# Kernel tuning notes

Measured on AMD Instinct MI355X. Metric: run time of the kernel, lower is better.

The kernel has to match this reference:

```python
import jax, jax.numpy as jnp
import numpy as np

K = 512          # num_embeddings
D = 8            # latent_dim
DECAY = 0.99     # ema_decay
EPS = 1e-5


def setup_inputs() -> dict:
    key = jax.random.key(0)
    k1, k2 = jax.random.split(key)
    z = jax.random.normal(k1, (64, D, 64, 64), dtype=jnp.float32)
    # codebook initialized uniform(-1/K, 1/K) as in the torch module
    codebook = jax.random.uniform(k2, (K, D), dtype=jnp.float32,
                                  minval=-1.0 / K, maxval=1.0 / K)
    ema_cluster_size = jnp.zeros((K,), dtype=jnp.float32)
    ema_w = jnp.zeros((K, D), dtype=jnp.float32)
    return {"z": z, "codebook": codebook,
            "ema_cluster_size": ema_cluster_size, "ema_w": ema_w}


def reference(z, codebook, ema_cluster_size, ema_w):
    B, C, H, W = z.shape
    # (B, HW, C) flattened latents, matching z.view(B,C,-1).permute(0,2,1)
    flat = z.reshape(B, C, H * W).transpose(0, 2, 1)

    # cdist p=2: ||z||^2 - 2 z.e + ||e||^2, then sqrt (argmin unaffected,
    # but we keep the sqrt for faithfulness to torch.cdist)
    z_sq = jnp.sum(flat * flat, axis=-1, keepdims=True)        # (B, N, 1)
    e_sq = jnp.sum(codebook * codebook, axis=-1)               # (K,)
    dots = jnp.einsum('bnd,kd->bnk', flat, codebook)           # (B, N, K)
    distances = jnp.sqrt(jnp.maximum(z_sq - 2.0 * dots + e_sq, 0.0))

    indices = jnp.argmin(distances, axis=-1)                   # (B, N) int

    # embedding gather with the OLD codebook (as in the torch forward)
    z_q = codebook[indices]                                    # (B, N, D)
    z_q = z_q.transpose(0, 2, 1).reshape(B, C, H, W)

    commitment_loss = jnp.mean((jax.lax.stop_gradient(z_q) - z) ** 2)
    loss = commitment_loss  # use_ema=True branch

    # ---- EMA in-place codebook update (buffers) ----
    idx_flat = indices.reshape(-1)                             # (B*N,)
    inp_flat = flat.reshape(-1, C)                             # (B*N, D)
    counts = jax.ops.segment_sum(jnp.ones_like(idx_flat, dtype=z.dtype),
                                 idx_flat, num_segments=K)     # (K,)
    sums = jax.ops.segment_sum(inp_flat, idx_flat, num_segments=K)  # (K, D)

    new_cs = ema_cluster_size * DECAY + counts * (1.0 - DECAY)
    new_w = ema_w * DECAY + sums * (1.0 - DECAY)
    n = jnp.sum(new_cs)
    cs_smoothed = (new_cs + EPS) / (n + K * EPS) * n
    new_codebook = new_w / cs_smoothed[:, None]

    return z_q, loss, new_codebook, cs_smoothed, new_w
```

## Files before the change

kernel.cpp:

```cpp
#include <hip/hip_runtime.h>

constexpr int Kc   = 512;
constexpr int Dc   = 8;
constexpr int HWc  = 4096;
constexpr int CHWc = Dc * HWc;
constexpr int Mc   = 64 * HWc;
constexpr int TOTALc = Mc * Dc;

constexpr int REP      = 8;
constexpr int RSTRIDE  = 4616;
constexpr int ACC_FLOATS = REP * RSTRIDE;

__global__ __launch_bounds__(256) void vq_prep(const float* __restrict__ cb,
                                               float* __restrict__ ws) {
    const int tid = blockIdx.x * 256 + threadIdx.x;
    float4* w4 = (float4*)ws;
    for (int i = tid; i < ACC_FLOATS / 4; i += gridDim.x * 256)
        w4[i] = float4{0.f, 0.f, 0.f, 0.f};
    if (blockIdx.x == 0) {
        for (int k = threadIdx.x; k < Kc; k += 256) {
            float s = 0.f;
#pragma unroll
            for (int c = 0; c < Dc; ++c) {
                const float e = cb[k * Dc + c];
                s = fmaf(e, e, s);
            }
            ws[ACC_FLOATS + k] = s;
        }
    }
}

__global__ __launch_bounds__(512, 8) void vq_main(const float* __restrict__ z,
                                                  const float* __restrict__ cb,
                                                  const float* __restrict__ esq,
                                                  float* __restrict__ ws,
                                                  float* __restrict__ zq) {
    __shared__ float s_counts[Kc];
    __shared__ float s_sums[Kc * Dc];
    __shared__ float s_mn[512];
    __shared__ int   s_im[512];
    __shared__ float s_loss;

    const int t = threadIdx.x;
    for (int i = t; i < Kc; i += 512) s_counts[i] = 0.f;
    for (int i = t; i < Kc * Dc; i += 512) s_sums[i] = 0.f;
    if (t == 0) s_loss = 0.f;

    const int v = t & 255;
    const int half = __builtin_amdgcn_readfirstlane(t >> 8);
    const int k0   = half << 8;

    const int m = blockIdx.x * 256 + v;
    const int n = m & (HWc - 1);
    const int b = m >> 12;
    const float* zb = z + b * CHWc + n;

    float zv[Dc], zz[Dc];
#pragma unroll
    for (int c = 0; c < Dc; ++c) {
        zv[c] = zb[c * HWc];
        zz[c] = -2.0f * zv[c];
    }

    float mn = 3.4e38f;
    int   im = k0;
#pragma unroll 4
    for (int kk = 0; kk < 256; ++kk) {
        const int k = k0 + kk;
        float a = esq[k];
#pragma unroll
        for (int c = 0; c < Dc; ++c) {
            const float e = cb[k * Dc + c];
            a = fmaf(zz[c], e, a);
        }
        const bool cm = a < mn;
        mn = cm ? a : mn;
        im = cm ? k : im;
    }
    s_mn[t] = mn;
    s_im[t] = im;
    __syncthreads();

    if (t < 256) {
        const float mn0 = s_mn[t];
        const float mn1 = s_mn[t + 256];
        const int   im0 = s_im[t];
        const int   im1 = s_im[t + 256];
        const int im = (mn1 < mn0) ? im1 : im0;

        const float4* cb4 = (const float4*)cb;
        const float4 qa = cb4[im * 2], qb = cb4[im * 2 + 1];
        const float q[Dc] = {qa.x, qa.y, qa.z, qa.w, qb.x, qb.y, qb.z, qb.w};

        float* zqb = zq + b * CHWc + n;
        float lsum = 0.f;
#pragma unroll
        for (int c = 0; c < Dc; ++c) {
            zqb[c * HWc] = q[c];
            const float d = q[c] - zv[c];
            lsum = fmaf(d, d, lsum);
        }

        unsafeAtomicAdd(&s_counts[im], 1.0f);
#pragma unroll
        for (int c = 0; c < Dc; ++c)
            unsafeAtomicAdd(&s_sums[im * Dc + c], zv[c]);
        unsafeAtomicAdd(&s_loss, lsum);
    }
    __syncthreads();

    float* acc = ws + (blockIdx.x & (REP - 1)) * RSTRIDE;
    for (int i = t; i < Kc; i += 512) {
        const float val = s_counts[i];
        if (val != 0.f) unsafeAtomicAdd(&acc[i], val);
    }
    for (int i = t; i < Kc * Dc; i += 512) {
        const float val = s_sums[i];
        if (val != 0.f) unsafeAtomicAdd(&acc[512 + i], val);
    }
    if (t == 0) unsafeAtomicAdd(&acc[4608], s_loss);
}

__global__ __launch_bounds__(512) void vq_final(const float* __restrict__ ws,
                                                const float* __restrict__ ema_cs,
                                                const float* __restrict__ ema_w,
                                                float* __restrict__ out) {
    constexpr float DEC  = 0.99f;
    constexpr float OMD  = (float)(1.0 - 0.99);
    constexpr float EPSf = 1e-5f;
    constexpr float KEPS = (float)(512 * 1e-5);
    __shared__ float red[512];

    const int k = threadIdx.x;
    float cnt = 0.f;
#pragma unroll
    for (int r = 0; r < REP; ++r) cnt += ws[r * RSTRIDE + k];
    const float ncs = ema_cs[k] * DEC + cnt * OMD;
    red[k] = ncs;
    __syncthreads();
    for (int s = 256; s > 0; s >>= 1) {
        if (k < s) red[k] += red[k + s];
        __syncthreads();
    }
    const float n  = red[0];
    const float cs = (ncs + EPSf) / (n + KEPS) * n;

    float* out_loss = out + TOTALc;
    float* out_cb   = out + TOTALc + 1;
    float* out_cs   = out_cb + Kc * Dc;
    float* out_nw   = out_cs + Kc;

    out_cs[k] = cs;
#pragma unroll
    for (int c = 0; c < Dc; ++c) {
        float sm = 0.f;
#pragma unroll
        for (int r = 0; r < REP; ++r) sm += ws[r * RSTRIDE + 512 + k * Dc + c];
        const float nw = ema_w[k * Dc + c] * DEC + sm * OMD;
        out_nw[k * Dc + c] = nw;
        out_cb[k * Dc + c] = nw / cs;
    }
    if (k == 0) {
        float ls = 0.f;
#pragma unroll
        for (int r = 0; r < REP; ++r) ls += ws[r * RSTRIDE + 4608];
        out_loss[0] = ls * (1.0f / 2097152.0f);
    }
}

extern "C" void kernel_launch(void* const* d_in, const int* in_sizes, int n_in,
                              void* d_out, int out_size, void* d_ws, size_t ws_size,
                              hipStream_t stream) {
    const float* z      = (const float*)d_in[0];
    const float* cb     = (const float*)d_in[1];
    const float* ema_cs = (const float*)d_in[2];
    const float* ema_w  = (const float*)d_in[3];
    float* out = (float*)d_out;
    float* ws  = (float*)d_ws;

    vq_prep<<<32, 256, 0, stream>>>(cb, ws);
    vq_main<<<Mc / 256, 512, 0, stream>>>(z, cb, ws + ACC_FLOATS, ws, out);
    vq_final<<<1, 512, 0, stream>>>(ws, ema_cs, ema_w, out);
}
```

Before: 129.3 us.

## Register-block two latents per thread and split codebook into four groups

The main kernel now has each thread evaluate two latent vectors against a 128-entry slice of the codebook, with four thread groups covering all 512 codes, instead of one vector against 256 codes across two groups. Each codebook element loaded is therefore reused for two FMAs, cutting cache and LDS traffic per distance. The partial argmins are combined over four groups in shared memory, and z is reloaded in the epilogue rather than kept in registers. The finalize kernel also switches to coalesced element-wise loops over the sums, with cluster sizes shared through LDS.

```diff
diff --git a/kernel.cpp b/kernel.cpp
--- a/kernel.cpp
+++ b/kernel.cpp
@@ -37,8 +37,8 @@
                                                   float* __restrict__ zq) {
     __shared__ float s_counts[Kc];
     __shared__ float s_sums[Kc * Dc];
-    __shared__ float s_mn[512];
-    __shared__ int   s_im[512];
+    __shared__ float s_mn[4][256];
+    __shared__ int   s_im[4][256];
     __shared__ float s_loss;
 
     const int t = threadIdx.x;
@@ -46,65 +46,82 @@
     for (int i = t; i < Kc * Dc; i += 512) s_sums[i] = 0.f;
     if (t == 0) s_loss = 0.f;
 
-    const int v = t & 255;
-    const int half = __builtin_amdgcn_readfirstlane(t >> 8);
-    const int k0   = half << 8;
-
-    const int m = blockIdx.x * 256 + v;
-    const int n = m & (HWc - 1);
-    const int b = m >> 12;
-    const float* zb = z + b * CHWc + n;
-
-    float zv[Dc], zz[Dc];
+    const int vl = t & 127;
+    const int g  = __builtin_amdgcn_readfirstlane(t >> 7);
+    const int k0 = g << 7;
+
+    const int base = blockIdx.x * 256;
+    const int n0 = (base + vl) & (HWc - 1);
+    const int b  = base >> 12;
+    const float* zb = z + b * CHWc + n0;
+
+    float zz0[Dc], zz1[Dc];
 #pragma unroll
     for (int c = 0; c < Dc; ++c) {
-        zv[c] = zb[c * HWc];
-        zz[c] = -2.0f * zv[c];
-    }
-
-    float mn = 3.4e38f;
-    int   im = k0;
+        zz0[c] = -2.0f * zb[c * HWc];
+        zz1[c] = -2.0f * zb[c * HWc + 128];
+    }
+
+    float mn0 = 3.4e38f, mn1 = 3.4e38f;
+    int   i0 = k0, i1 = k0;
 #pragma unroll 4
-    for (int kk = 0; kk < 256; ++kk) {
+    for (int kk = 0; kk < 128; ++kk) {
         const int k = k0 + kk;
-        float a = esq[k];
+        float a0 = esq[k];
+        float a1 = a0;
 #pragma unroll
         for (int c = 0; c < Dc; ++c) {
             const float e = cb[k * Dc + c];
-            a = fmaf(zz[c], e, a);
-        }
-        const bool cm = a < mn;
-        mn = cm ? a : mn;
-        im = cm ? k : im;
-    }
-    s_mn[t] = mn;
-    s_im[t] = im;
+            a0 = fmaf(zz0[c], e, a0);
+            a1 = fmaf(zz1[c], e, a1);
+        }
+        const bool c0 = a0 < mn0;
+        mn0 = c0 ? a0 : mn0;
+        i0  = c0 ? k  : i0;
+        const bool c1 = a1 < mn1;
+        mn1 = c1 ? a1 : mn1;
+        i1  = c1 ? k  : i1;
+    }
+    s_mn[g][vl]       = mn0;
+    s_im[g][vl]       = i0;
+    s_mn[g][vl + 128] = mn1;
+    s_im[g][vl + 128] = i1;
     __syncthreads();
 
     if (t < 256) {
-        const float mn0 = s_mn[t];
-        const float mn1 = s_mn[t + 256];
-        const int   im0 = s_im[t];
-        const int   im1 = s_im[t + 256];
-        const int im = (mn1 < mn0) ? im1 : im0;
+        const int v = t;
+        float mn = s_mn[0][v];
+        int   im = s_im[0][v];
+#pragma unroll
+        for (int gg = 1; gg < 4; ++gg) {
+            const float m2 = s_mn[gg][v];
+            const int   j2 = s_im[gg][v];
+            const bool  c2 = m2 < mn;
+            mn = c2 ? m2 : mn;
+            im = c2 ? j2 : im;
+        }
 
         const float4* cb4 = (const float4*)cb;
         const float4 qa = cb4[im * 2], qb = cb4[im * 2 + 1];
         const float q[Dc] = {qa.x, qa.y, qa.z, qa.w, qb.x, qb.y, qb.z, qb.w};
 
-        float* zqb = zq + b * CHWc + n;
+        const int nv = (base + v) & (HWc - 1);
+        const float* zv = z + b * CHWc + nv;
+        float* zqv = zq + b * CHWc + nv;
         float lsum = 0.f;
+        float zr[Dc];
 #pragma unroll
         for (int c = 0; c < Dc; ++c) {
-            zqb[c * HWc] = q[c];
-            const float d = q[c] - zv[c];
+            zr[c] = zv[c * HWc];
+            zqv[c * HWc] = q[c];
+            const float d = q[c] - zr[c];
             lsum = fmaf(d, d, lsum);
         }
 
         unsafeAtomicAdd(&s_counts[im], 1.0f);
 #pragma unroll
         for (int c = 0; c < Dc; ++c)
-            unsafeAtomicAdd(&s_sums[im * Dc + c], zv[c]);
+            unsafeAtomicAdd(&s_sums[im * Dc + c], zr[c]);
         unsafeAtomicAdd(&s_loss, lsum);
     }
     __syncthreads();
@@ -130,37 +147,40 @@
     constexpr float EPSf = 1e-5f;
     constexpr float KEPS = (float)(512 * 1e-5);
     __shared__ float red[512];
-
-    const int k = threadIdx.x;
+    __shared__ float s_cs[512];
+
+    const int t = threadIdx.x;
     float cnt = 0.f;
 #pragma unroll
-    for (int r = 0; r < REP; ++r) cnt += ws[r * RSTRIDE + k];
-    const float ncs = ema_cs[k] * DEC + cnt * OMD;
-    red[k] = ncs;
+    for (int r = 0; r < REP; ++r) cnt += ws[r * RSTRIDE + t];
+    const float ncs = ema_cs[t] * DEC + cnt * OMD;
+    red[t] = ncs;
     __syncthreads();
     for (int s = 256; s > 0; s >>= 1) {
-        if (k < s) red[k] += red[k + s];
+        if (t < s) red[t] += red[t + s];
         __syncthreads();
     }
     const float n  = red[0];
     const float cs = (ncs + EPSf) / (n + KEPS) * n;
+    s_cs[t] = cs;
 
     float* out_loss = out + TOTALc;
     float* out_cb   = out + TOTALc + 1;
     float* out_cs   = out_cb + Kc * Dc;
     float* out_nw   = out_cs + Kc;
 
-    out_cs[k] = cs;
-#pragma unroll
-    for (int c = 0; c < Dc; ++c) {
+    out_cs[t] = cs;
+    __syncthreads();
+
+    for (int e = t; e < Kc * Dc; e += 512) {
         float sm = 0.f;
 #pragma unroll
-        for (int r = 0; r < REP; ++r) sm += ws[r * RSTRIDE + 512 + k * Dc + c];
-        const float nw = ema_w[k * Dc + c] * DEC + sm * OMD;
-        out_nw[k * Dc + c] = nw;
-        out_cb[k * Dc + c] = nw / cs;
-    }
-    if (k == 0) {
+        for (int r = 0; r < REP; ++r) sm += ws[r * RSTRIDE + 512 + e];
+        const float nw = ema_w[e] * DEC + sm * OMD;
+        out_nw[e] = nw;
+        out_cb[e] = nw / s_cs[e >> 3];
+    }
+    if (t == 0) {
         float ls = 0.f;
 #pragma unroll
         for (int r = 0; r < REP; ++r) ls += ws[r * RSTRIDE + 4608];
```

After: 112.4 us. 13.1% less time.
